# Kernel optimization log

Measured on AMD Instinct MI355X. Metric: run time of the kernel, lower is better.

Reference implementation:

```python
import jax, jax.numpy as jnp
import numpy as np

N_NODES = 100000
N_EDGES = 1600000
F = 128


def setup_inputs() -> dict:
    key = jax.random.key(0)
    ks = jax.random.split(key, 8)
    edge_src = jax.random.randint(ks[0], (N_EDGES,), 0, N_NODES, dtype=jnp.int32)
    edge_dst = jax.random.randint(ks[1], (N_EDGES,), 0, N_NODES, dtype=jnp.int32)
    edge_vals = jax.random.uniform(ks[2], (N_EDGES,), dtype=jnp.float32)
    feats = jax.random.normal(ks[3], (N_NODES, F), dtype=jnp.float32)
    s = 1.0 / np.sqrt(F)
    W1 = jax.random.normal(ks[4], (F, F), dtype=jnp.float32) * s
    b1 = jax.random.normal(ks[5], (F,), dtype=jnp.float32) * s
    W2 = jax.random.normal(ks[6], (F, F), dtype=jnp.float32) * s
    b2 = jax.random.normal(ks[7], (F,), dtype=jnp.float32) * s
    return {"edge_src": edge_src, "edge_dst": edge_dst, "edge_vals": edge_vals,
            "feats": feats, "W1": W1, "b1": b1, "W2": W2, "b2": b2}


def reference(edge_src, edge_dst, edge_vals, feats, W1, b1, W2, b2):
    # LE = L @ feats  (SpMM over COO edges: dst <- sum val * feats[src])
    msgs = edge_vals[:, None] * jnp.take(feats, edge_src, axis=0)  # [E, F]
    LE = jax.ops.segment_sum(msgs, edge_dst, num_segments=feats.shape[0])  # [N, F]
    # sf_E = (L + I) @ feats = LE + feats  (SelfLoop is identity)
    sf_E = LE + feats
    left_part = sf_E @ W1.T + b1          # W1(sf_E)
    E = LE * feats                        # torch.mul(LE, feats)
    right_part = E @ W2.T + b2            # W2(E)
    return left_part + right_part
```

## Files before the change

kernel.cpp:

```cpp
#include <hip/hip_runtime.h>

#define N_NODES 100000
#define N_EDGES 1600000
#define F 128
#define M_PAD 100032
#define NCB 1563
#define CAP 2048
#define EPB 4096
#define FB_BLOCKS 25000
#define W_BLOCKS 64
#define CC_BLOCKS 7

typedef __attribute__((ext_vector_type(8))) short short8;
typedef __attribute__((ext_vector_type(4))) float float4v;

__device__ __forceinline__ unsigned pack_bf16(float x, float y) {
    unsigned ux = __float_as_uint(x), uy = __float_as_uint(y);
    ux = (ux + 0x7fffu + ((ux >> 16) & 1u)) >> 16;
    uy = (uy + 0x7fffu + ((uy >> 16) & 1u)) >> 16;
    return ux | (uy << 16);
}

__global__ __launch_bounds__(256) void prep_kernel(
    const float2* __restrict__ feats2, unsigned* __restrict__ featsb,
    const float* __restrict__ W1, const float* __restrict__ W2,
    unsigned* __restrict__ Wbu, int* __restrict__ ccur)
{
    int b = blockIdx.x, t = threadIdx.x;
    if (b < FB_BLOCKS) {
        int i = b * 256 + t;
        float2 v = feats2[i];
        featsb[i] = pack_bf16(v.x, v.y);
    } else if (b < FB_BLOCKS + W_BLOCKS) {
        int i = (b - FB_BLOCKS) * 256 + t;
        int j = i >> 7, c = i & 127;
        const float* s = (c < 64) ? &W1[j * 128 + 2 * c] : &W2[j * 128 + 2 * (c - 64)];
        Wbu[i] = pack_bf16(s[0], s[1]);
    } else {
        int i = (b - FB_BLOCKS - W_BLOCKS) * 256 + t;
        if (i < NCB) ccur[i] = i * CAP;
    }
}

__global__ __launch_bounds__(256) void passA_kernel(
    const int* __restrict__ esrc, const int* __restrict__ edst,
    const float* __restrict__ evals, int* __restrict__ ccur,
    int2* __restrict__ srtA)
{
    __shared__ int2 sv[EPB];
    __shared__ unsigned short bkt[EPB];
    __shared__ int h[NCB], lo[NCB], gbase[NCB];

    const int t = threadIdx.x;
    const int base = blockIdx.x * EPB;
    const int cnt = min(EPB, N_EDGES - base);

    for (int i = t; i < NCB; i += 256) h[i] = 0;
    __syncthreads();

    int rsrc[16], rdst[16], rrank[16];
    float rval[16];
#pragma unroll
    for (int i = 0; i < 16; i++) {
        int e = base + i * 256 + t;
        if (e < N_EDGES) {
            rsrc[i] = esrc[e];
            rdst[i] = edst[e];
            rval[i] = evals[e];
            rrank[i] = atomicAdd(&h[rdst[i] >> 6], 1);
        } else rdst[i] = -1;
    }
    __syncthreads();

    if (t < 64) {
        int carry = 0;
        for (int b0 = 0; b0 < NCB; b0 += 64) {
            int i = b0 + t;
            int x = (i < NCB) ? h[i] : 0;
            int v = x;
#pragma unroll
            for (int d = 1; d < 64; d <<= 1) {
                int y = __shfl_up(v, d);
                if (t >= d) v += y;
            }
            if (i < NCB) lo[i] = v - x + carry;
            carry += __shfl(v, 63);
        }
    }
    __syncthreads();

#pragma unroll
    for (int i = 0; i < 16; i++) {
        if (rdst[i] >= 0) {
            int b = rdst[i] >> 6;
            int s = lo[b] + rrank[i];
            sv[s]  = make_int2(rsrc[i] | ((rdst[i] & 63) << 24),
                               __float_as_int(rval[i]));
            bkt[s] = (unsigned short)b;
        }
    }
    for (int b = t; b < NCB; b += 256) {
        int c = h[b];
        if (c) gbase[b] = atomicAdd(&ccur[b], c);
    }
    __syncthreads();

    for (int s = t; s < cnt; s += 256) {
        int b = bkt[s];
        srtA[gbase[b] + (s - lo[b])] = sv[s];
    }
}

__global__ __launch_bounds__(256) void fused_gather_kernel(
    const int* __restrict__ ccur, const int2* __restrict__ srtA,
    const uint2* __restrict__ fb2,
    uint2* __restrict__ Abig2)
{
    __shared__ int2 list[CAP];
    __shared__ int hist[64], cur[64];

    const int t = threadIdx.x;
    const int b = blockIdx.x;
    const int base = b * CAP;
    const int cnt = ccur[b] - base;

    if (t < 64) hist[t] = 0;
    __syncthreads();

    for (int i = t; i < cnt; i += 256)
        atomicAdd(&hist[(unsigned)srtA[base + i].x >> 24], 1);
    __syncthreads();

    if (t < 64) {
        int x = hist[t], v = x;
#pragma unroll
        for (int d = 1; d < 64; d <<= 1) {
            int y = __shfl_up(v, d);
            if (t >= d) v += y;
        }
        cur[t] = v - x;
    }
    __syncthreads();

    for (int i = t; i < cnt; i += 256) {
        int2 e = srtA[base + i];
        int d = (unsigned)e.x >> 24;
        int pos = atomicAdd(&cur[d], 1);
        list[pos] = make_int2(e.x & 0x00FFFFFF, e.y);
    }
    __syncthreads();

    const int w = t >> 6;
    const int lane = t & 63;
    const int h = lane >> 5;
    const int l = lane & 31;

#pragma unroll
    for (int np = 0; np < 16; np += 2) {
        const int nl = w * 16 + np + h;
        const int end = cur[nl];
        int i = end - hist[nl];

        float a0 = 0.f, a1 = 0.f, a2 = 0.f, a3 = 0.f;
        for (; i + 3 < end; i += 4) {
            int2 e0 = list[i], e1 = list[i + 1], e2 = list[i + 2], e3 = list[i + 3];
            uint2 p0 = fb2[(size_t)e0.x * 32 + l];
            uint2 p1 = fb2[(size_t)e1.x * 32 + l];
            uint2 p2 = fb2[(size_t)e2.x * 32 + l];
            uint2 p3 = fb2[(size_t)e3.x * 32 + l];
            float v0 = __int_as_float(e0.y), v1 = __int_as_float(e1.y);
            float v2 = __int_as_float(e2.y), v3 = __int_as_float(e3.y);
            a0 += v0 * __uint_as_float(p0.x << 16) + v1 * __uint_as_float(p1.x << 16)
                + v2 * __uint_as_float(p2.x << 16) + v3 * __uint_as_float(p3.x << 16);
            a1 += v0 * __uint_as_float(p0.x & 0xffff0000u) + v1 * __uint_as_float(p1.x & 0xffff0000u)
                + v2 * __uint_as_float(p2.x & 0xffff0000u) + v3 * __uint_as_float(p3.x & 0xffff0000u);
            a2 += v0 * __uint_as_float(p0.y << 16) + v1 * __uint_as_float(p1.y << 16)
                + v2 * __uint_as_float(p2.y << 16) + v3 * __uint_as_float(p3.y << 16);
            a3 += v0 * __uint_as_float(p0.y & 0xffff0000u) + v1 * __uint_as_float(p1.y & 0xffff0000u)
                + v2 * __uint_as_float(p2.y & 0xffff0000u) + v3 * __uint_as_float(p3.y & 0xffff0000u);
        }
        for (; i < end; i++) {
            int2 e0 = list[i];
            uint2 p0 = fb2[(size_t)e0.x * 32 + l];
            float v0 = __int_as_float(e0.y);
            a0 += v0 * __uint_as_float(p0.x << 16);
            a1 += v0 * __uint_as_float(p0.x & 0xffff0000u);
            a2 += v0 * __uint_as_float(p0.y << 16);
            a3 += v0 * __uint_as_float(p0.y & 0xffff0000u);
        }

        const int gn = b * 64 + nl;
        if (gn < N_NODES) {
            uint2 pf = fb2[(size_t)gn * 32 + l];
            float f0 = __uint_as_float(pf.x << 16);
            float f1 = __uint_as_float(pf.x & 0xffff0000u);
            float f2v = __uint_as_float(pf.y << 16);
            float f3 = __uint_as_float(pf.y & 0xffff0000u);

            uint2 S, P;
            S.x = pack_bf16(a0 + f0, a1 + f1);  S.y = pack_bf16(a2 + f2v, a3 + f3);
            P.x = pack_bf16(a0 * f0, a1 * f1);  P.y = pack_bf16(a2 * f2v, a3 * f3);
            Abig2[(size_t)gn * 64 + l]      = S;
            Abig2[(size_t)gn * 64 + 32 + l] = P;
        }
    }
}

__global__ __launch_bounds__(256) void gemm_kernel(
    const unsigned short* __restrict__ Abig, const unsigned short* __restrict__ Wb,
    const float* __restrict__ b1, const float* __restrict__ b2,
    float* __restrict__ out)
{
    const int t = threadIdx.x;
    const int w = t >> 6, lane = t & 63;
    const int col = lane & 15;
    const int quad = lane >> 4;
    const int ko = quad * 8;
    const int m0 = blockIdx.x * 64 + w * 16;

    float4v acc[8];
#pragma unroll
    for (int j = 0; j < 8; j++) acc[j] = (float4v)(0.f);

    const unsigned short* arow = Abig + (size_t)(m0 + col) * 256 + ko;
#pragma unroll
    for (int k0 = 0; k0 < 8; k0++) {
        short8 a = *(const short8*)(arow + k0 * 32);
#pragma unroll
        for (int j = 0; j < 8; j++) {
            short8 b = *(const short8*)&Wb[(size_t)(j * 16 + col) * 256 + k0 * 32 + ko];
            acc[j] = __builtin_amdgcn_mfma_f32_16x16x32_bf16(a, b, acc[j], 0, 0, 0);
        }
    }

#pragma unroll
    for (int j = 0; j < 8; j++) {
        int n0 = j * 16 + col;
        float bb = b1[n0] + b2[n0];
#pragma unroll
        for (int r = 0; r < 4; r++) {
            int m = m0 + quad * 4 + r;
            if (m < N_NODES)
                __builtin_nontemporal_store(acc[j][r] + bb, &out[(size_t)m * F + n0]);
        }
    }
}

extern "C" void kernel_launch(void* const* d_in, const int* in_sizes, int n_in,
                              void* d_out, int out_size, void* d_ws, size_t ws_size,
                              hipStream_t stream) {
    const int*   edge_src  = (const int*)d_in[0];
    const int*   edge_dst  = (const int*)d_in[1];
    const float* edge_vals = (const float*)d_in[2];
    const float* feats     = (const float*)d_in[3];
    const float* W1        = (const float*)d_in[4];
    const float* b1        = (const float*)d_in[5];
    const float* W2        = (const float*)d_in[6];
    const float* b2        = (const float*)d_in[7];
    float* out = (float*)d_out;

    char* ws = (char*)d_ws;
    unsigned*       featsb = (unsigned*)      (ws);
    int2*           srtA   = (int2*)          (ws + 25600000);
    int*            ccur   = (int*)           (ws + 51208192);
    unsigned*       Wbu    = (unsigned*)      (ws + 51216384);
    unsigned short* Abig   = (unsigned short*)(ws + 51281920);

    prep_kernel<<<FB_BLOCKS + W_BLOCKS + CC_BLOCKS, 256, 0, stream>>>(
        (const float2*)feats, featsb, W1, W2, Wbu, ccur);

    passA_kernel<<<(N_EDGES + EPB - 1) / EPB, 256, 0, stream>>>(
        edge_src, edge_dst, edge_vals, ccur, srtA);

    fused_gather_kernel<<<NCB, 256, 0, stream>>>(
        ccur, srtA, (const uint2*)featsb, (uint2*)Abig);

    gemm_kernel<<<M_PAD / 64, 256, 0, stream>>>(
        Abig, (const unsigned short*)Wbu, b1, b2, out);
}
```

Before: 279.4 us.

## Fuse bf16 prep into bucketing kernel, memset counters, register-cache edges in gather

The standalone prep kernel is folded into the edge-bucketing kernel as extra blocks, so feature and weight bf16 conversion run alongside the sort. The bucket counters are zeroed with a memset and now hold relative counts rather than absolute offsets. The gather kernel keeps each thread's edges in registers between the histogram and scatter passes, avoiding a second global read, and adds an 8-wide unrolled gather loop for more loads in flight. The trade-offs are higher register pressure and an extra memset launch, in exchange for removing one kernel launch and one pass over the sorted edges.

```diff
diff --git a/kernel.cpp b/kernel.cpp
--- a/kernel.cpp
+++ b/kernel.cpp
@@ -7,9 +7,9 @@
 #define NCB 1563
 #define CAP 2048
 #define EPB 4096
+#define MS_BLOCKS 391
 #define FB_BLOCKS 25000
 #define W_BLOCKS 64
-#define CC_BLOCKS 7
 
 typedef __attribute__((ext_vector_type(8))) short short8;
 typedef __attribute__((ext_vector_type(4))) float float4v;
@@ -21,38 +21,37 @@
     return ux | (uy << 16);
 }
 
-__global__ __launch_bounds__(256) void prep_kernel(
-    const float2* __restrict__ feats2, unsigned* __restrict__ featsb,
-    const float* __restrict__ W1, const float* __restrict__ W2,
-    unsigned* __restrict__ Wbu, int* __restrict__ ccur)
-{
-    int b = blockIdx.x, t = threadIdx.x;
-    if (b < FB_BLOCKS) {
-        int i = b * 256 + t;
-        float2 v = feats2[i];
-        featsb[i] = pack_bf16(v.x, v.y);
-    } else if (b < FB_BLOCKS + W_BLOCKS) {
-        int i = (b - FB_BLOCKS) * 256 + t;
-        int j = i >> 7, c = i & 127;
-        const float* s = (c < 64) ? &W1[j * 128 + 2 * c] : &W2[j * 128 + 2 * (c - 64)];
-        Wbu[i] = pack_bf16(s[0], s[1]);
-    } else {
-        int i = (b - FB_BLOCKS - W_BLOCKS) * 256 + t;
-        if (i < NCB) ccur[i] = i * CAP;
-    }
-}
-
 __global__ __launch_bounds__(256) void passA_kernel(
     const int* __restrict__ esrc, const int* __restrict__ edst,
     const float* __restrict__ evals, int* __restrict__ ccur,
-    int2* __restrict__ srtA)
+    int2* __restrict__ srtA,
+    const float2* __restrict__ feats2, unsigned* __restrict__ featsb,
+    const float* __restrict__ W1, const float* __restrict__ W2,
+    unsigned* __restrict__ Wbu)
 {
     __shared__ int2 sv[EPB];
     __shared__ unsigned short bkt[EPB];
-    __shared__ int h[NCB], lo[NCB], gbase[NCB];
-
+    __shared__ int h[NCB], lo[NCB];
+
+    const int blk = blockIdx.x;
     const int t = threadIdx.x;
-    const int base = blockIdx.x * EPB;
+
+    if (blk >= MS_BLOCKS) {
+        int cb = blk - MS_BLOCKS;
+        if (cb < FB_BLOCKS) {
+            int i = cb * 256 + t;
+            float2 v = feats2[i];
+            featsb[i] = pack_bf16(v.x, v.y);
+        } else {
+            int i = (cb - FB_BLOCKS) * 256 + t;
+            int j = i >> 7, c = i & 127;
+            const float* s = (c < 64) ? &W1[j * 128 + 2 * c] : &W2[j * 128 + 2 * (c - 64)];
+            Wbu[i] = pack_bf16(s[0], s[1]);
+        }
+        return;
+    }
+
+    const int base = blk * EPB;
     const int cnt = min(EPB, N_EDGES - base);
 
     for (int i = t; i < NCB; i += 256) h[i] = 0;
@@ -99,16 +98,19 @@
             bkt[s] = (unsigned short)b;
         }
     }
+    __syncthreads();
+
     for (int b = t; b < NCB; b += 256) {
         int c = h[b];
-        if (c) gbase[b] = atomicAdd(&ccur[b], c);
-    }
-    __syncthreads();
-
-    for (int s = t; s < cnt; s += 256) {
-        int b = bkt[s];
-        srtA[gbase[b] + (s - lo[b])] = sv[s];
-    }
+        if (c) {
+            int g = b * CAP + atomicAdd(&ccur[b], c);
+            lo[b] = g - lo[b];
+        }
+    }
+    __syncthreads();
+
+    for (int s = t; s < cnt; s += 256)
+        srtA[lo[bkt[s]] + s] = sv[s];
 }
 
 __global__ __launch_bounds__(256) void fused_gather_kernel(
@@ -122,13 +124,22 @@
     const int t = threadIdx.x;
     const int b = blockIdx.x;
     const int base = b * CAP;
-    const int cnt = ccur[b] - base;
+    const int cnt = ccur[b];
 
     if (t < 64) hist[t] = 0;
     __syncthreads();
 
-    for (int i = t; i < cnt; i += 256)
-        atomicAdd(&hist[(unsigned)srtA[base + i].x >> 24], 1);
+    int2 r[8];
+    int rd[8];
+#pragma unroll
+    for (int k = 0; k < 8; k++) {
+        int i = t + k * 256;
+        if (i < cnt) {
+            r[k] = srtA[base + i];
+            rd[k] = (unsigned)r[k].x >> 24;
+            atomicAdd(&hist[rd[k]], 1);
+        } else rd[k] = -1;
+    }
     __syncthreads();
 
     if (t < 64) {
@@ -142,26 +153,43 @@
     }
     __syncthreads();
 
-    for (int i = t; i < cnt; i += 256) {
-        int2 e = srtA[base + i];
-        int d = (unsigned)e.x >> 24;
-        int pos = atomicAdd(&cur[d], 1);
-        list[pos] = make_int2(e.x & 0x00FFFFFF, e.y);
+#pragma unroll
+    for (int k = 0; k < 8; k++) {
+        if (rd[k] >= 0) {
+            int pos = atomicAdd(&cur[rd[k]], 1);
+            list[pos] = make_int2(r[k].x & 0x00FFFFFF, r[k].y);
+        }
     }
     __syncthreads();
 
     const int w = t >> 6;
     const int lane = t & 63;
-    const int h = lane >> 5;
+    const int hh = lane >> 5;
     const int l = lane & 31;
 
 #pragma unroll
     for (int np = 0; np < 16; np += 2) {
-        const int nl = w * 16 + np + h;
+        const int nl = w * 16 + np + hh;
         const int end = cur[nl];
         int i = end - hist[nl];
 
         float a0 = 0.f, a1 = 0.f, a2 = 0.f, a3 = 0.f;
+        for (; i + 7 < end; i += 8) {
+            int2 e[8];
+#pragma unroll
+            for (int k = 0; k < 8; k++) e[k] = list[i + k];
+            uint2 p[8];
+#pragma unroll
+            for (int k = 0; k < 8; k++) p[k] = fb2[(size_t)e[k].x * 32 + l];
+#pragma unroll
+            for (int k = 0; k < 8; k++) {
+                float v = __int_as_float(e[k].y);
+                a0 += v * __uint_as_float(p[k].x << 16);
+                a1 += v * __uint_as_float(p[k].x & 0xffff0000u);
+                a2 += v * __uint_as_float(p[k].y << 16);
+                a3 += v * __uint_as_float(p[k].y & 0xffff0000u);
+            }
+        }
         for (; i + 3 < end; i += 4) {
             int2 e0 = list[i], e1 = list[i + 1], e2 = list[i + 2], e3 = list[i + 3];
             uint2 p0 = fb2[(size_t)e0.x * 32 + l];
@@ -266,11 +294,11 @@
     unsigned*       Wbu    = (unsigned*)      (ws + 51216384);
     unsigned short* Abig   = (unsigned short*)(ws + 51281920);
 
-    prep_kernel<<<FB_BLOCKS + W_BLOCKS + CC_BLOCKS, 256, 0, stream>>>(
-        (const float2*)feats, featsb, W1, W2, Wbu, ccur);
-
-    passA_kernel<<<(N_EDGES + EPB - 1) / EPB, 256, 0, stream>>>(
-        edge_src, edge_dst, edge_vals, ccur, srtA);
+    hipMemsetAsync(ccur, 0, NCB * sizeof(int), stream);
+
+    passA_kernel<<<MS_BLOCKS + FB_BLOCKS + W_BLOCKS, 256, 0, stream>>>(
+        edge_src, edge_dst, edge_vals, ccur, srtA,
+        (const float2*)feats, featsb, W1, W2, Wbu);
 
     fused_gather_kernel<<<NCB, 256, 0, stream>>>(
         ccur, srtA, (const uint2*)featsb, (uint2*)Abig);
```

New measurement: 293.8 us. +5.1%, slower.

## Fuse SpMM gather and dual-weight GEMM into one kernel via LDS tile

Applied to the files above, without the earlier changes.

The gather kernel now writes its bf16 [sf_E | LE*feats] rows into a padded 64x264 shared-memory tile and runs the MFMA GEMM straight from LDS. This removes the separate GEMM launch and the global round trip of the 51 MB intermediate matrix. The feats-to-bf16 conversion is widened to 16-byte loads and stores, and passA folds the bucket base into the lo array instead of keeping a separate gbase array. The cost is much higher LDS use per block (about 50 KB), which may lower occupancy in the gather phase.

```diff
diff --git a/kernel.cpp b/kernel.cpp
--- a/kernel.cpp
+++ b/kernel.cpp
@@ -3,13 +3,14 @@
 #define N_NODES 100000
 #define N_EDGES 1600000
 #define F 128
-#define M_PAD 100032
 #define NCB 1563
 #define CAP 2048
 #define EPB 4096
-#define FB_BLOCKS 25000
+#define MS_BLOCKS 391
+#define FB_BLOCKS 6250
 #define W_BLOCKS 64
 #define CC_BLOCKS 7
+#define APAD 264
 
 typedef __attribute__((ext_vector_type(8))) short short8;
 typedef __attribute__((ext_vector_type(4))) float float4v;
@@ -22,15 +23,16 @@
 }
 
 __global__ __launch_bounds__(256) void prep_kernel(
-    const float2* __restrict__ feats2, unsigned* __restrict__ featsb,
+    const float4* __restrict__ feats4, uint4* __restrict__ featsb4,
     const float* __restrict__ W1, const float* __restrict__ W2,
     unsigned* __restrict__ Wbu, int* __restrict__ ccur)
 {
     int b = blockIdx.x, t = threadIdx.x;
     if (b < FB_BLOCKS) {
         int i = b * 256 + t;
-        float2 v = feats2[i];
-        featsb[i] = pack_bf16(v.x, v.y);
+        float4 v0 = feats4[2 * i], v1 = feats4[2 * i + 1];
+        featsb4[i] = make_uint4(pack_bf16(v0.x, v0.y), pack_bf16(v0.z, v0.w),
+                                pack_bf16(v1.x, v1.y), pack_bf16(v1.z, v1.w));
     } else if (b < FB_BLOCKS + W_BLOCKS) {
         int i = (b - FB_BLOCKS) * 256 + t;
         int j = i >> 7, c = i & 127;
@@ -38,7 +40,7 @@
         Wbu[i] = pack_bf16(s[0], s[1]);
     } else {
         int i = (b - FB_BLOCKS - W_BLOCKS) * 256 + t;
-        if (i < NCB) ccur[i] = i * CAP;
+        if (i < NCB) ccur[i] = 0;
     }
 }
 
@@ -49,7 +51,7 @@
 {
     __shared__ int2 sv[EPB];
     __shared__ unsigned short bkt[EPB];
-    __shared__ int h[NCB], lo[NCB], gbase[NCB];
+    __shared__ int h[NCB], lo[NCB];
 
     const int t = threadIdx.x;
     const int base = blockIdx.x * EPB;
@@ -99,30 +101,36 @@
             bkt[s] = (unsigned short)b;
         }
     }
+    __syncthreads();
+
     for (int b = t; b < NCB; b += 256) {
         int c = h[b];
-        if (c) gbase[b] = atomicAdd(&ccur[b], c);
-    }
-    __syncthreads();
-
-    for (int s = t; s < cnt; s += 256) {
-        int b = bkt[s];
-        srtA[gbase[b] + (s - lo[b])] = sv[s];
-    }
-}
-
-__global__ __launch_bounds__(256) void fused_gather_kernel(
+        if (c) {
+            int g = b * CAP + atomicAdd(&ccur[b], c);
+            lo[b] = g - lo[b];
+        }
+    }
+    __syncthreads();
+
+    for (int s = t; s < cnt; s += 256)
+        srtA[lo[bkt[s]] + s] = sv[s];
+}
+
+__global__ __launch_bounds__(256) void fused_kernel(
     const int* __restrict__ ccur, const int2* __restrict__ srtA,
     const uint2* __restrict__ fb2,
-    uint2* __restrict__ Abig2)
+    const unsigned short* __restrict__ Wb,
+    const float* __restrict__ b1, const float* __restrict__ b2,
+    float* __restrict__ out)
 {
     __shared__ int2 list[CAP];
+    __shared__ unsigned short Amat[64][APAD];
     __shared__ int hist[64], cur[64];
 
     const int t = threadIdx.x;
     const int b = blockIdx.x;
     const int base = b * CAP;
-    const int cnt = ccur[b] - base;
+    const int cnt = ccur[b];
 
     if (t < 64) hist[t] = 0;
     __syncthreads();
@@ -152,12 +160,12 @@
 
     const int w = t >> 6;
     const int lane = t & 63;
-    const int h = lane >> 5;
+    const int hh = lane >> 5;
     const int l = lane & 31;
 
 #pragma unroll
     for (int np = 0; np < 16; np += 2) {
-        const int nl = w * 16 + np + h;
+        const int nl = w * 16 + np + hh;
         const int end = cur[nl];
         int i = end - hist[nl];
 
@@ -190,56 +198,48 @@
         }
 
         const int gn = b * 64 + nl;
-        if (gn < N_NODES) {
-            uint2 pf = fb2[(size_t)gn * 32 + l];
-            float f0 = __uint_as_float(pf.x << 16);
-            float f1 = __uint_as_float(pf.x & 0xffff0000u);
-            float f2v = __uint_as_float(pf.y << 16);
-            float f3 = __uint_as_float(pf.y & 0xffff0000u);
-
-            uint2 S, P;
-            S.x = pack_bf16(a0 + f0, a1 + f1);  S.y = pack_bf16(a2 + f2v, a3 + f3);
-            P.x = pack_bf16(a0 * f0, a1 * f1);  P.y = pack_bf16(a2 * f2v, a3 * f3);
-            Abig2[(size_t)gn * 64 + l]      = S;
-            Abig2[(size_t)gn * 64 + 32 + l] = P;
-        }
-    }
-}
-
-__global__ __launch_bounds__(256) void gemm_kernel(
-    const unsigned short* __restrict__ Abig, const unsigned short* __restrict__ Wb,
-    const float* __restrict__ b1, const float* __restrict__ b2,
-    float* __restrict__ out)
-{
-    const int t = threadIdx.x;
-    const int w = t >> 6, lane = t & 63;
+        uint2 pf = make_uint2(0u, 0u);
+        if (gn < N_NODES) pf = fb2[(size_t)gn * 32 + l];
+        float f0 = __uint_as_float(pf.x << 16);
+        float f1 = __uint_as_float(pf.x & 0xffff0000u);
+        float f2v = __uint_as_float(pf.y << 16);
+        float f3 = __uint_as_float(pf.y & 0xffff0000u);
+
+        uint2 S, P;
+        S.x = pack_bf16(a0 + f0, a1 + f1);  S.y = pack_bf16(a2 + f2v, a3 + f3);
+        P.x = pack_bf16(a0 * f0, a1 * f1);  P.y = pack_bf16(a2 * f2v, a3 * f3);
+        *(uint2*)&Amat[nl][4 * l]       = S;
+        *(uint2*)&Amat[nl][128 + 4 * l] = P;
+    }
+    __syncthreads();
+
     const int col = lane & 15;
     const int quad = lane >> 4;
     const int ko = quad * 8;
-    const int m0 = blockIdx.x * 64 + w * 16;
+    const int r0 = w * 16;
 
     float4v acc[8];
 #pragma unroll
     for (int j = 0; j < 8; j++) acc[j] = (float4v)(0.f);
 
-    const unsigned short* arow = Abig + (size_t)(m0 + col) * 256 + ko;
 #pragma unroll
     for (int k0 = 0; k0 < 8; k0++) {
-        short8 a = *(const short8*)(arow + k0 * 32);
+        short8 a = *(const short8*)&Amat[r0 + col][k0 * 32 + ko];
 #pragma unroll
         for (int j = 0; j < 8; j++) {
-            short8 b = *(const short8*)&Wb[(size_t)(j * 16 + col) * 256 + k0 * 32 + ko];
-            acc[j] = __builtin_amdgcn_mfma_f32_16x16x32_bf16(a, b, acc[j], 0, 0, 0);
-        }
-    }
-
+            short8 bw = *(const short8*)&Wb[(j * 16 + col) * 256 + k0 * 32 + ko];
+            acc[j] = __builtin_amdgcn_mfma_f32_16x16x32_bf16(a, bw, acc[j], 0, 0, 0);
+        }
+    }
+
+    const int gm0 = b * 64 + r0;
 #pragma unroll
     for (int j = 0; j < 8; j++) {
         int n0 = j * 16 + col;
         float bb = b1[n0] + b2[n0];
 #pragma unroll
         for (int r = 0; r < 4; r++) {
-            int m = m0 + quad * 4 + r;
+            int m = gm0 + quad * 4 + r;
             if (m < N_NODES)
                 __builtin_nontemporal_store(acc[j][r] + bb, &out[(size_t)m * F + n0]);
         }
@@ -264,17 +264,13 @@
     int2*           srtA   = (int2*)          (ws + 25600000);
     int*            ccur   = (int*)           (ws + 51208192);
     unsigned*       Wbu    = (unsigned*)      (ws + 51216384);
-    unsigned short* Abig   = (unsigned short*)(ws + 51281920);
 
     prep_kernel<<<FB_BLOCKS + W_BLOCKS + CC_BLOCKS, 256, 0, stream>>>(
-        (const float2*)feats, featsb, W1, W2, Wbu, ccur);
-
-    passA_kernel<<<(N_EDGES + EPB - 1) / EPB, 256, 0, stream>>>(
+        (const float4*)feats, (uint4*)featsb, W1, W2, Wbu, ccur);
+
+    passA_kernel<<<MS_BLOCKS, 256, 0, stream>>>(
         edge_src, edge_dst, edge_vals, ccur, srtA);
 
-    fused_gather_kernel<<<NCB, 256, 0, stream>>>(
-        ccur, srtA, (const uint2*)featsb, (uint2*)Abig);
-
-    gemm_kernel<<<M_PAD / 64, 256, 0, stream>>>(
-        Abig, (const unsigned short*)Wbu, b1, b2, out);
-}
+    fused_kernel<<<NCB, 256, 0, stream>>>(
+        ccur, srtA, (const uint2*)featsb, (const unsigned short*)Wbu, b1, b2, out);
+}
```

Result: slower. 288.6 us (+3.3%).

## Use 128-node destination buckets, vectorize bf16 prep, simplify scatter offsets

Applied to the files above, without the earlier changes.

Destination buckets grow from 64 to 128 nodes, which halves the bucket count in the edge-sorting pass and the number of gather blocks. Each gather block now processes 32 nodes per wave with a two-chunk prefix scan. The feature-to-bf16 conversion now handles 8 floats per thread with 128-bit loads and stores. The scatter folds the global base into the local offset table, which removes the gbase array. Fewer, larger gather blocks may reduce occupancy and load balance, and bucket capacity is now fixed at 2432 edges per bucket.

```diff
diff --git a/kernel.cpp b/kernel.cpp
--- a/kernel.cpp
+++ b/kernel.cpp
@@ -4,12 +4,13 @@
 #define N_EDGES 1600000
 #define F 128
 #define M_PAD 100032
-#define NCB 1563
-#define CAP 2048
+#define NCB 782
+#define CAP 2432
 #define EPB 4096
-#define FB_BLOCKS 25000
+#define MS_BLOCKS 391
+#define FB_BLOCKS 6250
 #define W_BLOCKS 64
-#define CC_BLOCKS 7
+#define CC_BLOCKS 4
 
 typedef __attribute__((ext_vector_type(8))) short short8;
 typedef __attribute__((ext_vector_type(4))) float float4v;
@@ -22,15 +23,16 @@
 }
 
 __global__ __launch_bounds__(256) void prep_kernel(
-    const float2* __restrict__ feats2, unsigned* __restrict__ featsb,
+    const float4* __restrict__ feats4, uint4* __restrict__ featsb4,
     const float* __restrict__ W1, const float* __restrict__ W2,
     unsigned* __restrict__ Wbu, int* __restrict__ ccur)
 {
     int b = blockIdx.x, t = threadIdx.x;
     if (b < FB_BLOCKS) {
         int i = b * 256 + t;
-        float2 v = feats2[i];
-        featsb[i] = pack_bf16(v.x, v.y);
+        float4 v0 = feats4[2 * i], v1 = feats4[2 * i + 1];
+        featsb4[i] = make_uint4(pack_bf16(v0.x, v0.y), pack_bf16(v0.z, v0.w),
+                                pack_bf16(v1.x, v1.y), pack_bf16(v1.z, v1.w));
     } else if (b < FB_BLOCKS + W_BLOCKS) {
         int i = (b - FB_BLOCKS) * 256 + t;
         int j = i >> 7, c = i & 127;
@@ -49,7 +51,7 @@
 {
     __shared__ int2 sv[EPB];
     __shared__ unsigned short bkt[EPB];
-    __shared__ int h[NCB], lo[NCB], gbase[NCB];
+    __shared__ int h[NCB], lo[NCB];
 
     const int t = threadIdx.x;
     const int base = blockIdx.x * EPB;
@@ -67,7 +69,7 @@
             rsrc[i] = esrc[e];
             rdst[i] = edst[e];
             rval[i] = evals[e];
-            rrank[i] = atomicAdd(&h[rdst[i] >> 6], 1);
+            rrank[i] = atomicAdd(&h[rdst[i] >> 7], 1);
         } else rdst[i] = -1;
     }
     __syncthreads();
@@ -92,23 +94,26 @@
 #pragma unroll
     for (int i = 0; i < 16; i++) {
         if (rdst[i] >= 0) {
-            int b = rdst[i] >> 6;
+            int b = rdst[i] >> 7;
             int s = lo[b] + rrank[i];
-            sv[s]  = make_int2(rsrc[i] | ((rdst[i] & 63) << 24),
+            sv[s]  = make_int2(rsrc[i] | ((rdst[i] & 127) << 24),
                                __float_as_int(rval[i]));
             bkt[s] = (unsigned short)b;
         }
     }
+    __syncthreads();
+
     for (int b = t; b < NCB; b += 256) {
         int c = h[b];
-        if (c) gbase[b] = atomicAdd(&ccur[b], c);
-    }
-    __syncthreads();
-
-    for (int s = t; s < cnt; s += 256) {
-        int b = bkt[s];
-        srtA[gbase[b] + (s - lo[b])] = sv[s];
-    }
+        if (c) {
+            int g = atomicAdd(&ccur[b], c);
+            lo[b] = g - lo[b];
+        }
+    }
+    __syncthreads();
+
+    for (int s = t; s < cnt; s += 256)
+        srtA[lo[bkt[s]] + s] = sv[s];
 }
 
 __global__ __launch_bounds__(256) void fused_gather_kernel(
@@ -117,14 +122,14 @@
     uint2* __restrict__ Abig2)
 {
     __shared__ int2 list[CAP];
-    __shared__ int hist[64], cur[64];
+    __shared__ int hist[128], cur[128];
 
     const int t = threadIdx.x;
     const int b = blockIdx.x;
     const int base = b * CAP;
     const int cnt = ccur[b] - base;
 
-    if (t < 64) hist[t] = 0;
+    if (t < 128) hist[t] = 0;
     __syncthreads();
 
     for (int i = t; i < cnt; i += 256)
@@ -132,13 +137,19 @@
     __syncthreads();
 
     if (t < 64) {
-        int x = hist[t], v = x;
-#pragma unroll
-        for (int d = 1; d < 64; d <<= 1) {
-            int y = __shfl_up(v, d);
-            if (t >= d) v += y;
-        }
-        cur[t] = v - x;
+        int carry = 0;
+#pragma unroll
+        for (int c = 0; c < 2; c++) {
+            int i = c * 64 + t;
+            int x = hist[i], v = x;
+#pragma unroll
+            for (int d = 1; d < 64; d <<= 1) {
+                int y = __shfl_up(v, d);
+                if (t >= d) v += y;
+            }
+            cur[i] = v - x + carry;
+            carry += __shfl(v, 63);
+        }
     }
     __syncthreads();
 
@@ -152,12 +163,11 @@
 
     const int w = t >> 6;
     const int lane = t & 63;
-    const int h = lane >> 5;
+    const int hh = lane >> 5;
     const int l = lane & 31;
 
-#pragma unroll
-    for (int np = 0; np < 16; np += 2) {
-        const int nl = w * 16 + np + h;
+    for (int np = 0; np < 32; np += 2) {
+        const int nl = w * 32 + np + hh;
         const int end = cur[nl];
         int i = end - hist[nl];
 
@@ -189,7 +199,7 @@
             a3 += v0 * __uint_as_float(p0.y & 0xffff0000u);
         }
 
-        const int gn = b * 64 + nl;
+        const int gn = b * 128 + nl;
         if (gn < N_NODES) {
             uint2 pf = fb2[(size_t)gn * 32 + l];
             float f0 = __uint_as_float(pf.x << 16);
@@ -262,14 +272,14 @@
     char* ws = (char*)d_ws;
     unsigned*       featsb = (unsigned*)      (ws);
     int2*           srtA   = (int2*)          (ws + 25600000);
-    int*            ccur   = (int*)           (ws + 51208192);
-    unsigned*       Wbu    = (unsigned*)      (ws + 51216384);
-    unsigned short* Abig   = (unsigned short*)(ws + 51281920);
+    int*            ccur   = (int*)           (ws + 40814592);
+    unsigned*       Wbu    = (unsigned*)      (ws + 40818688);
+    unsigned short* Abig   = (unsigned short*)(ws + 40884224);
 
     prep_kernel<<<FB_BLOCKS + W_BLOCKS + CC_BLOCKS, 256, 0, stream>>>(
-        (const float2*)feats, featsb, W1, W2, Wbu, ccur);
-
-    passA_kernel<<<(N_EDGES + EPB - 1) / EPB, 256, 0, stream>>>(
+        (const float4*)feats, (uint4*)featsb, W1, W2, Wbu, ccur);
+
+    passA_kernel<<<MS_BLOCKS, 256, 0, stream>>>(
         edge_src, edge_dst, edge_vals, ccur, srtA);
 
     fused_gather_kernel<<<NCB, 256, 0, stream>>>(
```

Result: no change. 277.2 us (-0.8%).
